# Optimization experiments

Measured on AMD Instinct MI355X. Metric: run time of the kernel, lower is better.

The kernel has to match this reference:

```python
import jax, jax.numpy as jnp
import numpy as np
from jax.scipy.special import logsumexp

B, T = 64, 1024
NF, NH = 512, 512
NK = 500          # n_kcs (chains)
NS = 2            # n_states == n_outputs == 2


def setup_inputs() -> dict:
    key = jax.random.key(0)
    ks = jax.random.split(key, 8)
    return {
        "corr": jax.random.randint(ks[0], (B, T), 0, 2),
        "kc": jax.random.randint(ks[1], (B, T), 0, NK),
        "FM": jax.random.normal(ks[2], (B, T, NF), dtype=jnp.float32),
        "W1": jax.random.normal(ks[3], (NF, NH), jnp.float32) / np.sqrt(NF).astype(np.float32),
        "b1": jnp.zeros((NH,), jnp.float32),
        "W2": jax.random.normal(ks[4], (NH, 2), jnp.float32) / np.sqrt(NH).astype(np.float32),
        "b2": jnp.zeros((2,), jnp.float32),
        "trans_logits": jax.random.normal(ks[5], (NK, NS, NS), jnp.float32),
        "obs_logits": jax.random.normal(ks[6], (NK, NS, 2), jnp.float32),
        "init_logits": jax.random.normal(ks[7], (NK, NS), jnp.float32),
    }


def _bkt_forward(corr, kc, FM, W1, b1, W2, b2, trans_logits, obs_logits, init_logits):
    # MLP producing per-timestep observation logit features
    h = jnp.tanh(FM @ W1 + b1)                 # [B,T,NH]
    o = h @ W2 + b2                            # [B,T,2] (one per state)
    fv = jnp.stack([o, -o], axis=3)            # [B,T,NS,2] == cat((o, -o), dim=3)

    n_batch = corr.shape[0]
    bidx = jnp.arange(n_batch)
    log_t = jax.nn.log_softmax(trans_logits, axis=1)          # [NK,NS,NS], softmax over dim 1
    la0 = jnp.tile(jax.nn.log_softmax(init_logits, axis=1)[None], (n_batch, 1, 1))  # [B,NK,NS]

    def step(la_all, xs):
        y, c, fv_t = xs                         # y:[B] obs, c:[B] chain, fv_t:[B,NS,2]
        log_obs = jax.nn.log_softmax(obs_logits[c] + fv_t, axis=2)   # [B,NS,2]
        la = la_all[bidx, c]                    # [B,NS] gather current chain alpha
        log_py = logsumexp(log_obs + la[:, :, None], axis=1)         # [B,2]
        log_py = log_py - logsumexp(log_py, axis=1, keepdims=True)
        # emission prob of observed symbol per state: log_obs[b,:,y[b]]
        lp = jnp.take_along_axis(log_obs, y[:, None, None], axis=2)[..., 0]  # [B,NS]
        new_la = logsumexp(lp[:, None, :] + la[:, None, :] + log_t[c], axis=2)  # [B,NS]
        la_all = la_all.at[bidx, c].set(new_la)
        return la_all, log_py

    xs = (corr.T, kc.T, jnp.moveaxis(fv, 1, 0))   # time-major for scan
    _, outs = jax.lax.scan(step, la0, xs)         # outs: [T,B,2]
    return jnp.transpose(outs, (1, 0, 2))         # [B,T,2]


def reference(corr, kc, FM, W1, b1, W2, b2, trans_logits, obs_logits, init_logits):
    return _bkt_forward(corr, kc, FM, W1, b1, W2, b2, trans_logits, obs_logits, init_logits)
```

## Files before the change

kernel.cpp:

```cpp
#include <hip/hip_runtime.h>
#include <hip/hip_bf16.h>
#include <stdint.h>

typedef unsigned short u16;
typedef __bf16 bf16x8 __attribute__((ext_vector_type(8)));
typedef float floatx4 __attribute__((ext_vector_type(4)));

#define B_SZ 64
#define T_SZ 1024
#define NK 500

__device__ __forceinline__ u16 f2bf(float f) {
    union { float f; uint32_t u; } v; v.f = f;
    uint32_t u = v.u;
    u += 0x7FFFu + ((u >> 16) & 1u);
    return (u16)(u >> 16);
}

__device__ __forceinline__ float exp2_hw(float x) { return __builtin_amdgcn_exp2f(x); }
__device__ __forceinline__ float log2_hw(float x) { return __builtin_amdgcn_logf(x); }

__device__ __forceinline__ float lse2(float a, float b) {
    float m = fmaxf(a, b);
    float d = fabsf(a - b);
    return fmaf(0.6931471805599453f,
                log2_hw(1.0f + exp2_hw(-d * 1.4426950408889634f)), m);
}

__device__ __forceinline__ void load_lds16(const void* g, void* s) {
    __builtin_amdgcn_global_load_lds(
        (const __attribute__((address_space(1))) void*)g,
        (__attribute__((address_space(3))) void*)s, 16, 0, 0);
}

__global__ __launch_bounds__(256) void transpose_cvt(const float* __restrict__ in,
                                                     u16* __restrict__ out) {
    __shared__ float tile[32][33];
    int tx = threadIdx.x, ty = threadIdx.y;
    int x = blockIdx.x * 32 + tx;
    int y0 = blockIdx.y * 32 + ty;
    for (int i = 0; i < 32; i += 8)
        tile[ty + i][tx] = in[(size_t)(y0 + i) * 512 + x];
    __syncthreads();
    int x2 = blockIdx.y * 32 + tx;
    int y2 = blockIdx.x * 32 + ty;
    for (int i = 0; i < 32; i += 8)
        out[(size_t)(y2 + i) * 512 + x2] = f2bf(tile[tx][ty + i]);
}

__global__ __launch_bounds__(256, 2) void mlp_fused(
    const float* __restrict__ FM, const u16* __restrict__ W1T,
    const float* __restrict__ b1, const float* __restrict__ W2,
    const float* __restrict__ b2, float* __restrict__ o_buf) {

    __shared__ __align__(16) u16 ldsA[64 * 512];
    __shared__ __align__(16) u16 ldsB[256 * 32];
    float* ldsO = (float*)ldsB;

    const int tid  = threadIdx.x;
    const int w    = tid >> 6;
    const int lane = tid & 63;
    const int col  = lane & 15;
    const int g    = lane >> 4;
    const size_t row0 = (size_t)blockIdx.x * 64;

#pragma unroll
    for (int i = 0; i < 16; ++i) {
        int flat = i * 256 + tid;
        int row  = flat >> 6;
        int k8   = flat & 63;
        const float* src = FM + (row0 + row) * 512 + k8 * 8;
        float4 f0 = ((const float4*)src)[0];
        float4 f1 = ((const float4*)src)[1];
        union { uint4 v; u16 s[8]; } p;
        p.s[0] = f2bf(f0.x); p.s[1] = f2bf(f0.y);
        p.s[2] = f2bf(f0.z); p.s[3] = f2bf(f0.w);
        p.s[4] = f2bf(f1.x); p.s[5] = f2bf(f1.y);
        p.s[6] = f2bf(f1.z); p.s[7] = f2bf(f1.w);
        int sw = k8 ^ (row & 7);
        *(uint4*)(ldsA + row * 512 + sw * 8) = p.v;
    }

    float po[4][4][2];
#pragma unroll
    for (int mi = 0; mi < 4; mi++)
#pragma unroll
        for (int r = 0; r < 4; r++) { po[mi][r][0] = 0.f; po[mi][r][1] = 0.f; }

    for (int chunk = 0; chunk < 2; ++chunk) {
        floatx4 acc[4][4];
        floatx4 zero = {0.f, 0.f, 0.f, 0.f};
#pragma unroll
        for (int mi = 0; mi < 4; mi++)
#pragma unroll
            for (int ni = 0; ni < 4; ni++) acc[mi][ni] = zero;

        for (int ks = 0; ks < 16; ++ks) {
#pragma unroll
            for (int j = 0; j < 4; ++j) {
                int idx = j * 256 + tid;
                int nb  = idx >> 6;
                int gg  = (idx >> 4) & 3;
                int cc  = idx & 15;
                const u16* gsrc = W1T + (size_t)(chunk * 256 + nb * 16 + cc) * 512
                                       + ks * 32 + gg * 8;
                load_lds16(gsrc, ldsB + idx * 8);
            }
            __syncthreads();

            bf16x8 afr[4], bfr[4];
#pragma unroll
            for (int mi = 0; mi < 4; mi++) {
                int sw = (ks * 4 + g) ^ (col & 7);
                afr[mi] = *(const bf16x8*)(ldsA + (mi * 16 + col) * 512 + sw * 8);
            }
#pragma unroll
            for (int ni = 0; ni < 4; ni++)
                bfr[ni] = *(const bf16x8*)(ldsB + ((w * 4 + ni) * 64 + g * 16 + col) * 8);
#pragma unroll
            for (int mi = 0; mi < 4; mi++)
#pragma unroll
                for (int ni = 0; ni < 4; ni++)
                    acc[mi][ni] = __builtin_amdgcn_mfma_f32_16x16x32_bf16(
                        afr[mi], bfr[ni], acc[mi][ni], 0, 0, 0);
            __syncthreads();
        }

#pragma unroll
        for (int ni = 0; ni < 4; ni++) {
            int n = chunk * 256 + w * 64 + ni * 16 + col;
            float b1f = b1[n];
            float w20 = W2[2 * n], w21 = W2[2 * n + 1];
#pragma unroll
            for (int mi = 0; mi < 4; mi++)
#pragma unroll
                for (int r = 0; r < 4; r++) {
                    float x = acc[mi][ni][r] + b1f;
                    float ax = fabsf(x);
                    float e = exp2_hw(-2.885390082f * ax);
                    float t = (1.f - e) / (1.f + e);
                    float h = copysignf(t, x);
                    po[mi][r][0] += h * w20;
                    po[mi][r][1] += h * w21;
                }
        }
    }

#pragma unroll
    for (int mi = 0; mi < 4; mi++)
#pragma unroll
        for (int r = 0; r < 4; r++)
#pragma unroll
            for (int j = 0; j < 2; j++) {
                float v = po[mi][r][j];
                v += __shfl_xor(v, 1, 64);
                v += __shfl_xor(v, 2, 64);
                v += __shfl_xor(v, 4, 64);
                v += __shfl_xor(v, 8, 64);
                po[mi][r][j] = v;
            }
    __syncthreads();
    if (col == 0) {
#pragma unroll
        for (int mi = 0; mi < 4; mi++)
#pragma unroll
            for (int r = 0; r < 4; r++) {
                int row = mi * 16 + g * 4 + r;
                ldsO[(row * 4 + w) * 2 + 0] = po[mi][r][0];
                ldsO[(row * 4 + w) * 2 + 1] = po[mi][r][1];
            }
    }
    __syncthreads();
    if (tid < 128) {
        int row = tid >> 1, j = tid & 1;
        float v = ldsO[(row * 4 + 0) * 2 + j] + ldsO[(row * 4 + 1) * 2 + j]
                + ldsO[(row * 4 + 2) * 2 + j] + ldsO[(row * 4 + 3) * 2 + j] + b2[j];
        o_buf[(row0 + row) * 2 + j] = v;
    }
}

__global__ __launch_bounds__(64) void bkt_scan(
    const int* __restrict__ corr, const int* __restrict__ kc,
    const float* __restrict__ trans_logits,
    const float* __restrict__ obs_logits,
    const float* __restrict__ init_logits,
    const float* __restrict__ o_buf,
    float* __restrict__ out) {

    __shared__ int s_kc[T_SZ];
    __shared__ int s_corr[T_SZ];
    __shared__ float2 s_o[T_SZ];
    const int b = blockIdx.x >> 3;
    const int g = blockIdx.x & 7;
    const int lane = threadIdx.x;

#pragma unroll
    for (int i = 0; i < 4; ++i) {
        int t4 = i * 64 + lane;
        ((int4*)s_kc)[t4]   = ((const int4*)(kc + b * T_SZ))[t4];
        ((int4*)s_corr)[t4] = ((const int4*)(corr + b * T_SZ))[t4];
    }
#pragma unroll
    for (int i = 0; i < 8; ++i) {
        int t4 = i * 64 + lane;
        ((float4*)s_o)[t4] = ((const float4*)(o_buf + (size_t)b * T_SZ * 2))[t4];
    }
    __syncthreads();

    const int c  = g * 64 + lane;
    const int cp = c < NK ? c : NK - 1;

    float ob00 = obs_logits[cp * 4 + 0], ob01 = obs_logits[cp * 4 + 1];
    float ob10 = obs_logits[cp * 4 + 2], ob11 = obs_logits[cp * 4 + 3];
    float tr00 = trans_logits[cp * 4 + 0], tr01 = trans_logits[cp * 4 + 1];
    float tr10 = trans_logits[cp * 4 + 2], tr11 = trans_logits[cp * 4 + 3];
    float n0 = lse2(tr00, tr10), n1 = lse2(tr01, tr11);
    float lt00 = tr00 - n0, lt01 = tr01 - n1;
    float lt10 = tr10 - n0, lt11 = tr11 - n1;
    float i0 = init_logits[cp * 2], i1 = init_logits[cp * 2 + 1];
    float nli = lse2(i0, i1);
    float la0 = i0 - nli, la1 = i1 - nli;

    for (int w16 = 0; w16 < 16; ++w16) {
        int tl = w16 * 64 + lane;
        unsigned long long mask = __ballot((s_kc[tl] >> 6) == g);
        while (mask) {
            int tz = __builtin_ctzll(mask);
            mask &= mask - 1;
            int t = w16 * 64 + tz;
            int kct = s_kc[t];
            if (c == kct) {
                float o0 = s_o[t].x, o1 = s_o[t].y;
                float x00 = ob00 + o0, x01 = ob01 - o0;
                float x10 = ob10 + o1, x11 = ob11 - o1;
                float d0 = lse2(x00, x01), d1 = lse2(x10, x11);
                float lo00 = x00 - d0, lo01 = x01 - d0;
                float lo10 = x10 - d1, lo11 = x11 - d1;
                float py0 = lse2(lo00 + la0, lo10 + la1);
                float py1 = lse2(lo01 + la0, lo11 + la1);
                float pn = lse2(py0, py1);
                ((float2*)out)[(size_t)b * T_SZ + t] = make_float2(py0 - pn, py1 - pn);
                float lp0 = s_corr[t] ? lo01 : lo00;
                float lp1 = s_corr[t] ? lo11 : lo10;
                float t0 = lp0 + la0, t1 = lp1 + la1;
                float nla0 = lse2(t0 + lt00, t1 + lt01);
                float nla1 = lse2(t0 + lt10, t1 + lt11);
                la0 = nla0; la1 = nla1;
            }
        }
    }
}

extern "C" void kernel_launch(void* const* d_in, const int* in_sizes, int n_in,
                              void* d_out, int out_size, void* d_ws, size_t ws_size,
                              hipStream_t stream) {
    const int*   corr = (const int*)d_in[0];
    const int*   kc   = (const int*)d_in[1];
    const float* FM   = (const float*)d_in[2];
    const float* W1   = (const float*)d_in[3];
    const float* b1   = (const float*)d_in[4];
    const float* W2   = (const float*)d_in[5];
    const float* b2   = (const float*)d_in[6];
    const float* trans_logits = (const float*)d_in[7];
    const float* obs_logits   = (const float*)d_in[8];
    const float* init_logits  = (const float*)d_in[9];
    float* out = (float*)d_out;

    u16*   w1t   = (u16*)d_ws;
    float* o_buf = (float*)((char*)d_ws + 512 * 512 * 2);

    transpose_cvt<<<dim3(16, 16), dim3(32, 8), 0, stream>>>(W1, w1t);
    mlp_fused<<<1024, 256, 0, stream>>>(FM, w1t, b1, W2, b2, o_buf);
    bkt_scan<<<B_SZ * 8, 64, 0, stream>>>(corr, kc, trans_logits, obs_logits,
                                          init_logits, o_buf, out);
}
```

Baseline: 329.1 us.

## Load W1 fragments directly to registers with double buffering, drop LDS B staging

The MLP GEMM no longer stages W1T tiles through LDS with per-k-step barriers. Each wave now loads its B fragments straight from global (L2-resident) memory into registers, double-buffered one k-step ahead. It also computes all 128 of its columns in one pass (acc[4][8]), replacing the previous two 256-column chunks. This removes 32 block barriers and the LDS round trip for B, so MFMA work overlaps the loads of the next k-step. The cost is higher register pressure (128 accumulator floats plus 16 bf16x8 buffers) and uncoalesced-ish global fragment loads, which could reduce occupancy under launch_bounds(256,2).

```diff
diff --git a/kernel.cpp b/kernel.cpp
--- a/kernel.cpp
+++ b/kernel.cpp
@@ -25,12 +25,6 @@
     float d = fabsf(a - b);
     return fmaf(0.6931471805599453f,
                 log2_hw(1.0f + exp2_hw(-d * 1.4426950408889634f)), m);
-}
-
-__device__ __forceinline__ void load_lds16(const void* g, void* s) {
-    __builtin_amdgcn_global_load_lds(
-        (const __attribute__((address_space(1))) void*)g,
-        (__attribute__((address_space(3))) void*)s, 16, 0, 0);
 }
 
 __global__ __launch_bounds__(256) void transpose_cvt(const float* __restrict__ in,
@@ -54,8 +48,7 @@
     const float* __restrict__ b2, float* __restrict__ o_buf) {
 
     __shared__ __align__(16) u16 ldsA[64 * 512];
-    __shared__ __align__(16) u16 ldsB[256 * 32];
-    float* ldsO = (float*)ldsB;
+    __shared__ float ldsO[64][4][2];
 
     const int tid  = threadIdx.x;
     const int w    = tid >> 6;
@@ -80,6 +73,57 @@
         int sw = k8 ^ (row & 7);
         *(uint4*)(ldsA + row * 512 + sw * 8) = p.v;
     }
+    __syncthreads();
+
+    const u16* bbase = W1T + (size_t)(w * 128 + col) * 512 + g * 8;
+
+    floatx4 acc[4][8];
+    floatx4 zero = {0.f, 0.f, 0.f, 0.f};
+#pragma unroll
+    for (int mi = 0; mi < 4; mi++)
+#pragma unroll
+        for (int ni = 0; ni < 8; ni++) acc[mi][ni] = zero;
+
+    bf16x8 bA[8], bB[8];
+#pragma unroll
+    for (int ni = 0; ni < 8; ni++)
+        bA[ni] = *(const bf16x8*)(bbase + ni * 16 * 512);
+
+    for (int ks2 = 0; ks2 < 16; ks2 += 2) {
+#pragma unroll
+        for (int ni = 0; ni < 8; ni++)
+            bB[ni] = *(const bf16x8*)(bbase + ni * 16 * 512 + (ks2 + 1) * 32);
+        {
+            bf16x8 afr[4];
+            int sw = (ks2 * 4 + g) ^ (col & 7);
+#pragma unroll
+            for (int mi = 0; mi < 4; mi++)
+                afr[mi] = *(const bf16x8*)(ldsA + (mi * 16 + col) * 512 + sw * 8);
+#pragma unroll
+            for (int mi = 0; mi < 4; mi++)
+#pragma unroll
+                for (int ni = 0; ni < 8; ni++)
+                    acc[mi][ni] = __builtin_amdgcn_mfma_f32_16x16x32_bf16(
+                        afr[mi], bA[ni], acc[mi][ni], 0, 0, 0);
+        }
+        int ksn = (ks2 + 2) & 15;
+#pragma unroll
+        for (int ni = 0; ni < 8; ni++)
+            bA[ni] = *(const bf16x8*)(bbase + ni * 16 * 512 + ksn * 32);
+        {
+            bf16x8 afr[4];
+            int sw = ((ks2 + 1) * 4 + g) ^ (col & 7);
+#pragma unroll
+            for (int mi = 0; mi < 4; mi++)
+                afr[mi] = *(const bf16x8*)(ldsA + (mi * 16 + col) * 512 + sw * 8);
+#pragma unroll
+            for (int mi = 0; mi < 4; mi++)
+#pragma unroll
+                for (int ni = 0; ni < 8; ni++)
+                    acc[mi][ni] = __builtin_amdgcn_mfma_f32_16x16x32_bf16(
+                        afr[mi], bB[ni], acc[mi][ni], 0, 0, 0);
+        }
+    }
 
     float po[4][4][2];
 #pragma unroll
@@ -87,63 +131,23 @@
 #pragma unroll
         for (int r = 0; r < 4; r++) { po[mi][r][0] = 0.f; po[mi][r][1] = 0.f; }
 
-    for (int chunk = 0; chunk < 2; ++chunk) {
-        floatx4 acc[4][4];
-        floatx4 zero = {0.f, 0.f, 0.f, 0.f};
+#pragma unroll
+    for (int ni = 0; ni < 8; ni++) {
+        int n = w * 128 + ni * 16 + col;
+        float b1f = b1[n];
+        float w20 = W2[2 * n], w21 = W2[2 * n + 1];
 #pragma unroll
         for (int mi = 0; mi < 4; mi++)
 #pragma unroll
-            for (int ni = 0; ni < 4; ni++) acc[mi][ni] = zero;
-
-        for (int ks = 0; ks < 16; ++ks) {
-#pragma unroll
-            for (int j = 0; j < 4; ++j) {
-                int idx = j * 256 + tid;
-                int nb  = idx >> 6;
-                int gg  = (idx >> 4) & 3;
-                int cc  = idx & 15;
-                const u16* gsrc = W1T + (size_t)(chunk * 256 + nb * 16 + cc) * 512
-                                       + ks * 32 + gg * 8;
-                load_lds16(gsrc, ldsB + idx * 8);
-            }
-            __syncthreads();
-
-            bf16x8 afr[4], bfr[4];
-#pragma unroll
-            for (int mi = 0; mi < 4; mi++) {
-                int sw = (ks * 4 + g) ^ (col & 7);
-                afr[mi] = *(const bf16x8*)(ldsA + (mi * 16 + col) * 512 + sw * 8);
-            }
-#pragma unroll
-            for (int ni = 0; ni < 4; ni++)
-                bfr[ni] = *(const bf16x8*)(ldsB + ((w * 4 + ni) * 64 + g * 16 + col) * 8);
-#pragma unroll
-            for (int mi = 0; mi < 4; mi++)
-#pragma unroll
-                for (int ni = 0; ni < 4; ni++)
-                    acc[mi][ni] = __builtin_amdgcn_mfma_f32_16x16x32_bf16(
-                        afr[mi], bfr[ni], acc[mi][ni], 0, 0, 0);
-            __syncthreads();
-        }
-
-#pragma unroll
-        for (int ni = 0; ni < 4; ni++) {
-            int n = chunk * 256 + w * 64 + ni * 16 + col;
-            float b1f = b1[n];
-            float w20 = W2[2 * n], w21 = W2[2 * n + 1];
-#pragma unroll
-            for (int mi = 0; mi < 4; mi++)
-#pragma unroll
-                for (int r = 0; r < 4; r++) {
-                    float x = acc[mi][ni][r] + b1f;
-                    float ax = fabsf(x);
-                    float e = exp2_hw(-2.885390082f * ax);
-                    float t = (1.f - e) / (1.f + e);
-                    float h = copysignf(t, x);
-                    po[mi][r][0] += h * w20;
-                    po[mi][r][1] += h * w21;
-                }
-        }
+            for (int r = 0; r < 4; r++) {
+                float x = acc[mi][ni][r] + b1f;
+                float ax = fabsf(x);
+                float e = exp2_hw(-2.885390082f * ax);
+                float t = (1.f - e) / (1.f + e);
+                float h = copysignf(t, x);
+                po[mi][r][0] += h * w20;
+                po[mi][r][1] += h * w21;
+            }
     }
 
 #pragma unroll
@@ -159,22 +163,21 @@
                 v += __shfl_xor(v, 8, 64);
                 po[mi][r][j] = v;
             }
-    __syncthreads();
     if (col == 0) {
 #pragma unroll
         for (int mi = 0; mi < 4; mi++)
 #pragma unroll
             for (int r = 0; r < 4; r++) {
                 int row = mi * 16 + g * 4 + r;
-                ldsO[(row * 4 + w) * 2 + 0] = po[mi][r][0];
-                ldsO[(row * 4 + w) * 2 + 1] = po[mi][r][1];
+                ldsO[row][w][0] = po[mi][r][0];
+                ldsO[row][w][1] = po[mi][r][1];
             }
     }
     __syncthreads();
     if (tid < 128) {
         int row = tid >> 1, j = tid & 1;
-        float v = ldsO[(row * 4 + 0) * 2 + j] + ldsO[(row * 4 + 1) * 2 + j]
-                + ldsO[(row * 4 + 2) * 2 + j] + ldsO[(row * 4 + 3) * 2 + j] + b2[j];
+        float v = ldsO[row][0][j] + ldsO[row][1][j]
+                + ldsO[row][2][j] + ldsO[row][3][j] + b2[j];
         o_buf[(row0 + row) * 2 + j] = v;
     }
 }
```

New measurement: 326.3 us. No clear change (-0.9%).

## Restructure MLP kernel: full-N 512-thread blocks with double-buffered W1 and streamed FM

Applied to the files above, without the earlier changes.

The fused MLP kernel now uses 512-thread blocks that cover all 512 hidden columns in one pass. Each block loops over four 64-row tiles of FM, which reuses W1 tiles across more rows and removes the two-chunk N loop. W1 k-slices are double-buffered in LDS so the load of the next slice overlaps the current MFMA step. The next FM tile is prefetched into registers and converted into LDS slice by slice while the current tile computes. The tanh division is replaced with a hardware reciprocal. In exchange, the grid shrinks to 256 blocks with higher LDS use per block, which may limit latency hiding. The MLP stage may also be a small share of total time next to the scan.

```diff
diff --git a/kernel.cpp b/kernel.cpp
--- a/kernel.cpp
+++ b/kernel.cpp
@@ -19,6 +19,7 @@
 
 __device__ __forceinline__ float exp2_hw(float x) { return __builtin_amdgcn_exp2f(x); }
 __device__ __forceinline__ float log2_hw(float x) { return __builtin_amdgcn_logf(x); }
+__device__ __forceinline__ float rcp_hw(float x)  { return __builtin_amdgcn_rcpf(x); }
 
 __device__ __forceinline__ float lse2(float a, float b) {
     float m = fmaxf(a, b);
@@ -48,28 +49,29 @@
         out[(size_t)(y2 + i) * 512 + x2] = f2bf(tile[tx][ty + i]);
 }
 
-__global__ __launch_bounds__(256, 2) void mlp_fused(
+__global__ __launch_bounds__(512, 2) void mlp_fused(
     const float* __restrict__ FM, const u16* __restrict__ W1T,
     const float* __restrict__ b1, const float* __restrict__ W2,
     const float* __restrict__ b2, float* __restrict__ o_buf) {
 
     __shared__ __align__(16) u16 ldsA[64 * 512];
-    __shared__ __align__(16) u16 ldsB[256 * 32];
-    float* ldsO = (float*)ldsB;
+    __shared__ __align__(16) u16 ldsB[2][512 * 32];
+    __shared__ float ldsO[64][8][2];
 
     const int tid  = threadIdx.x;
     const int w    = tid >> 6;
     const int lane = tid & 63;
     const int col  = lane & 15;
     const int g    = lane >> 4;
-    const size_t row0 = (size_t)blockIdx.x * 64;
-
-#pragma unroll
-    for (int i = 0; i < 16; ++i) {
-        int flat = i * 256 + tid;
+    const int bid  = blockIdx.x;
+    const size_t rowB = (size_t)bid * 256;
+
+#pragma unroll
+    for (int i = 0; i < 8; ++i) {
+        int flat = i * 512 + tid;
         int row  = flat >> 6;
         int k8   = flat & 63;
-        const float* src = FM + (row0 + row) * 512 + k8 * 8;
+        const float* src = FM + (rowB + row) * 512 + k8 * 8;
         float4 f0 = ((const float4*)src)[0];
         float4 f1 = ((const float4*)src)[1];
         union { uint4 v; u16 s[8]; } p;
@@ -77,105 +79,143 @@
         p.s[2] = f2bf(f0.z); p.s[3] = f2bf(f0.w);
         p.s[4] = f2bf(f1.x); p.s[5] = f2bf(f1.y);
         p.s[6] = f2bf(f1.z); p.s[7] = f2bf(f1.w);
-        int sw = k8 ^ (row & 7);
-        *(uint4*)(ldsA + row * 512 + sw * 8) = p.v;
-    }
-
-    float po[4][4][2];
+        *(uint4*)(ldsA + row * 512 + (k8 ^ (row & 7)) * 8) = p.v;
+    }
+#pragma unroll
+    for (int jj = 0; jj < 4; ++jj) {
+        int idx = jj * 512 + tid;
+        int nb = idx >> 6, gg = (idx >> 4) & 3, cc = idx & 15;
+        load_lds16(W1T + (size_t)(nb * 16 + cc) * 512 + gg * 8,
+                   &ldsB[0][idx * 8]);
+    }
+
+    const int arow = (tid & 255) >> 2;
+    const int ak8l = tid & 3;
+    float4 areg[2][2];
+
+    floatx4 acc[4][4];
+    floatx4 zero = {0.f, 0.f, 0.f, 0.f};
 #pragma unroll
     for (int mi = 0; mi < 4; mi++)
 #pragma unroll
-        for (int r = 0; r < 4; r++) { po[mi][r][0] = 0.f; po[mi][r][1] = 0.f; }
-
-    for (int chunk = 0; chunk < 2; ++chunk) {
-        floatx4 acc[4][4];
-        floatx4 zero = {0.f, 0.f, 0.f, 0.f};
-#pragma unroll
-        for (int mi = 0; mi < 4; mi++)
-#pragma unroll
-            for (int ni = 0; ni < 4; ni++) acc[mi][ni] = zero;
-
-        for (int ks = 0; ks < 16; ++ks) {
-#pragma unroll
-            for (int j = 0; j < 4; ++j) {
-                int idx = j * 256 + tid;
-                int nb  = idx >> 6;
-                int gg  = (idx >> 4) & 3;
-                int cc  = idx & 15;
-                const u16* gsrc = W1T + (size_t)(chunk * 256 + nb * 16 + cc) * 512
-                                       + ks * 32 + gg * 8;
-                load_lds16(gsrc, ldsB + idx * 8);
-            }
-            __syncthreads();
-
+        for (int ni = 0; ni < 4; ni++) acc[mi][ni] = zero;
+
+    for (int j = 0; j < 64; ++j) {
+        const int kt = j & 15;
+        __syncthreads();
+
+        if (j < 63) {
+            const int ksl = (j + 1) & 15;
+            u16* dst = ldsB[(j + 1) & 1];
+#pragma unroll
+            for (int jj = 0; jj < 4; ++jj) {
+                int idx = jj * 512 + tid;
+                int nb = idx >> 6, gg = (idx >> 4) & 3, cc = idx & 15;
+                load_lds16(W1T + (size_t)(nb * 16 + cc) * 512 + ksl * 32 + gg * 8,
+                           dst + idx * 8);
+            }
+        }
+
+        if (tid < 256) {
+            if (j >= 2 && j <= 49) {
+                int ks = (j - 2) & 15;
+                float4 f0 = areg[j & 1][0], f1 = areg[j & 1][1];
+                union { uint4 v; u16 s[8]; } p;
+                p.s[0] = f2bf(f0.x); p.s[1] = f2bf(f0.y);
+                p.s[2] = f2bf(f0.z); p.s[3] = f2bf(f0.w);
+                p.s[4] = f2bf(f1.x); p.s[5] = f2bf(f1.y);
+                p.s[6] = f2bf(f1.z); p.s[7] = f2bf(f1.w);
+                int k8 = ks * 4 + ak8l;
+                *(uint4*)(ldsA + arow * 512 + (k8 ^ (arow & 7)) * 8) = p.v;
+            }
+            if (j < 48) {
+                const float* src = FM + (rowB + (size_t)((j >> 4) + 1) * 64 + arow) * 512
+                                      + ((j & 15) * 4 + ak8l) * 8;
+                areg[j & 1][0] = ((const float4*)src)[0];
+                areg[j & 1][1] = ((const float4*)src)[1];
+            }
+        }
+
+        {
+            const u16* bbuf = ldsB[j & 1];
             bf16x8 afr[4], bfr[4];
 #pragma unroll
             for (int mi = 0; mi < 4; mi++) {
-                int sw = (ks * 4 + g) ^ (col & 7);
+                int sw = (kt * 4 + g) ^ (col & 7);
                 afr[mi] = *(const bf16x8*)(ldsA + (mi * 16 + col) * 512 + sw * 8);
             }
 #pragma unroll
             for (int ni = 0; ni < 4; ni++)
-                bfr[ni] = *(const bf16x8*)(ldsB + ((w * 4 + ni) * 64 + g * 16 + col) * 8);
+                bfr[ni] = *(const bf16x8*)(bbuf + ((w * 4 + ni) * 64 + g * 16 + col) * 8);
 #pragma unroll
             for (int mi = 0; mi < 4; mi++)
 #pragma unroll
                 for (int ni = 0; ni < 4; ni++)
                     acc[mi][ni] = __builtin_amdgcn_mfma_f32_16x16x32_bf16(
                         afr[mi], bfr[ni], acc[mi][ni], 0, 0, 0);
+        }
+
+        if (kt == 15) {
+            const int i = j >> 4;
+            float po[4][4][2];
+#pragma unroll
+            for (int mi = 0; mi < 4; mi++)
+#pragma unroll
+                for (int r = 0; r < 4; r++) { po[mi][r][0] = 0.f; po[mi][r][1] = 0.f; }
+#pragma unroll
+            for (int ni = 0; ni < 4; ni++) {
+                int n = w * 64 + ni * 16 + col;
+                float b1f = b1[n];
+                float w20 = W2[2 * n], w21 = W2[2 * n + 1];
+#pragma unroll
+                for (int mi = 0; mi < 4; mi++)
+#pragma unroll
+                    for (int r = 0; r < 4; r++) {
+                        float x = acc[mi][ni][r] + b1f;
+                        float ax = fabsf(x);
+                        float e = exp2_hw(-2.885390082f * ax);
+                        float t = (1.f - e) * rcp_hw(1.f + e);
+                        float h = copysignf(t, x);
+                        po[mi][r][0] += h * w20;
+                        po[mi][r][1] += h * w21;
+                    }
+            }
+#pragma unroll
+            for (int mi = 0; mi < 4; mi++)
+#pragma unroll
+                for (int r = 0; r < 4; r++)
+#pragma unroll
+                    for (int jj = 0; jj < 2; jj++) {
+                        float v = po[mi][r][jj];
+                        v += __shfl_xor(v, 1, 64);
+                        v += __shfl_xor(v, 2, 64);
+                        v += __shfl_xor(v, 4, 64);
+                        v += __shfl_xor(v, 8, 64);
+                        po[mi][r][jj] = v;
+                    }
+            if (col == 0) {
+#pragma unroll
+                for (int mi = 0; mi < 4; mi++)
+#pragma unroll
+                    for (int r = 0; r < 4; r++) {
+                        int row = mi * 16 + g * 4 + r;
+                        ldsO[row][w][0] = po[mi][r][0];
+                        ldsO[row][w][1] = po[mi][r][1];
+                    }
+            }
             __syncthreads();
-        }
-
-#pragma unroll
-        for (int ni = 0; ni < 4; ni++) {
-            int n = chunk * 256 + w * 64 + ni * 16 + col;
-            float b1f = b1[n];
-            float w20 = W2[2 * n], w21 = W2[2 * n + 1];
+            if (tid < 128) {
+                int row = tid >> 1, jo = tid & 1;
+                float v = b2[jo];
+#pragma unroll
+                for (int ww = 0; ww < 8; ww++) v += ldsO[row][ww][jo];
+                o_buf[(rowB + (size_t)i * 64 + row) * 2 + jo] = v;
+            }
 #pragma unroll
             for (int mi = 0; mi < 4; mi++)
 #pragma unroll
-                for (int r = 0; r < 4; r++) {
-                    float x = acc[mi][ni][r] + b1f;
-                    float ax = fabsf(x);
-                    float e = exp2_hw(-2.885390082f * ax);
-                    float t = (1.f - e) / (1.f + e);
-                    float h = copysignf(t, x);
-                    po[mi][r][0] += h * w20;
-                    po[mi][r][1] += h * w21;
-                }
-        }
-    }
-
-#pragma unroll
-    for (int mi = 0; mi < 4; mi++)
-#pragma unroll
-        for (int r = 0; r < 4; r++)
-#pragma unroll
-            for (int j = 0; j < 2; j++) {
-                float v = po[mi][r][j];
-                v += __shfl_xor(v, 1, 64);
-                v += __shfl_xor(v, 2, 64);
-                v += __shfl_xor(v, 4, 64);
-                v += __shfl_xor(v, 8, 64);
-                po[mi][r][j] = v;
-            }
-    __syncthreads();
-    if (col == 0) {
-#pragma unroll
-        for (int mi = 0; mi < 4; mi++)
-#pragma unroll
-            for (int r = 0; r < 4; r++) {
-                int row = mi * 16 + g * 4 + r;
-                ldsO[(row * 4 + w) * 2 + 0] = po[mi][r][0];
-                ldsO[(row * 4 + w) * 2 + 1] = po[mi][r][1];
-            }
-    }
-    __syncthreads();
-    if (tid < 128) {
-        int row = tid >> 1, j = tid & 1;
-        float v = ldsO[(row * 4 + 0) * 2 + j] + ldsO[(row * 4 + 1) * 2 + j]
-                + ldsO[(row * 4 + 2) * 2 + j] + ldsO[(row * 4 + 3) * 2 + j] + b2[j];
-        o_buf[(row0 + row) * 2 + j] = v;
+                for (int ni = 0; ni < 4; ni++) acc[mi][ni] = zero;
+        }
     }
 }
 
@@ -270,7 +310,7 @@
     float* o_buf = (float*)((char*)d_ws + 512 * 512 * 2);
 
     transpose_cvt<<<dim3(16, 16), dim3(32, 8), 0, stream>>>(W1, w1t);
-    mlp_fused<<<1024, 256, 0, stream>>>(FM, w1t, b1, W2, b2, o_buf);
+    mlp_fused<<<256, 512, 0, stream>>>(FM, w1t, b1, W2, b2, o_buf);
     bkt_scan<<<B_SZ * 8, 64, 0, stream>>>(corr, kc, trans_logits, obs_logits,
                                           init_logits, o_buf, out);
 }
```

Result: slower. 361.4 us (+9.8%).
